# Optimization experiments

Measured on AMD Instinct MI355X. Metric: run time of the kernel, lower is better.

The kernel has to match this reference:

```python
import jax, jax.numpy as jnp
import numpy as np
import math

B, S, D = 2, 2048, 1024
H, KV, HD = 16, 4, 64
N_REP = H // KV
ROPE_THETA = 1.0e6


def _rope_tables(seq_len, head_dim, theta):
    inv_freq = 1.0 / (theta ** (np.arange(0, head_dim, 2, dtype=np.float32) / head_dim))
    t = np.arange(seq_len, dtype=np.float32)
    freqs = np.outer(t, inv_freq)                      # [S, HD/2]
    emb = np.concatenate([freqs, freqs], axis=-1)      # [S, HD]
    return jnp.asarray(np.cos(emb)), jnp.asarray(np.sin(emb))


def setup_inputs() -> dict:
    key = jax.random.key(0)
    ks = jax.random.split(key, 6)
    cos, sin = _rope_tables(S, HD, ROPE_THETA)
    scale = 0.02
    return {
        "x": jax.random.normal(ks[0], (B, S, D), dtype=jnp.float32),
        "cos": cos,
        "sin": sin,
        "Wq": jax.random.normal(ks[1], (D, H * HD), dtype=jnp.float32) * scale,
        "Wk": jax.random.normal(ks[2], (D, KV * HD), dtype=jnp.float32) * scale,
        "Wv": jax.random.normal(ks[3], (D, KV * HD), dtype=jnp.float32) * scale,
        "Wo": jax.random.normal(ks[4], (H * HD, D), dtype=jnp.float32) * scale,
    }


def _rotate_half(u):
    u1, u2 = u[..., : HD // 2], u[..., HD // 2 :]
    return jnp.concatenate([-u2, u1], axis=-1)


def reference(x, cos, sin, Wq, Wk, Wv, Wo):
    bsz, seq_len, _ = x.shape
    q = (x @ Wq).reshape(bsz, seq_len, H, HD)   # [B,S,H,HD]
    k = (x @ Wk).reshape(bsz, seq_len, KV, HD)  # [B,S,KV,HD]
    v = (x @ Wv).reshape(bsz, seq_len, KV, HD)

    # RoPE: cos/sin [S,HD] broadcast over batch and heads (unsqueeze_dim=1)
    c = cos[:seq_len][None, :, None, :]
    s = sin[:seq_len][None, :, None, :]
    q = q * c + _rotate_half(q) * s
    k = k * c + _rotate_half(k) * s

    # repeat_kv: expand KV heads groupwise to H heads
    k = jnp.repeat(k, N_REP, axis=2)  # [B,S,H,HD]
    v = jnp.repeat(v, N_REP, axis=2)

    q = q.transpose(0, 2, 1, 3)  # [B,H,S,HD]
    k = k.transpose(0, 2, 1, 3)
    v = v.transpose(0, 2, 1, 3)

    scores = jnp.einsum("bhqd,bhkd->bhqk", q, k) / math.sqrt(HD)
    causal = jnp.tril(jnp.ones((seq_len, seq_len), dtype=bool))
    scores = jnp.where(causal[None, None], scores, jnp.finfo(jnp.float32).min)
    probs = jax.nn.softmax(scores.astype(jnp.float32), axis=-1).astype(x.dtype)

    out = jnp.einsum("bhqk,bhkd->bhqd", probs, v)        # [B,H,S,HD]
    out = out.transpose(0, 2, 1, 3).reshape(bsz, seq_len, H * HD)
    return out @ Wo
```

## Files before the change

### kernel.cpp

```cpp
#include <hip/hip_runtime.h>

#define SS 2048
#define NH 16
#define NKV 4
#define HD 64

typedef __bf16 bf16;
typedef __bf16 bf16x4 __attribute__((ext_vector_type(4)));
typedef __bf16 bf16x8 __attribute__((ext_vector_type(8)));
typedef float f32x4 __attribute__((ext_vector_type(4)));

#define SM_SCALE 0.18033688011f

__device__ __forceinline__ void gl_lds16(const bf16* g, bf16* l) {
    __builtin_amdgcn_global_load_lds((const __attribute__((address_space(1))) void*)g,
                                     (__attribute__((address_space(3))) void*)l, 16, 0, 0);
}

__global__ __launch_bounds__(256) void prep_kernel(
    const float* __restrict__ x,
    const float* __restrict__ Wq, const float* __restrict__ Wk,
    const float* __restrict__ Wv, const float* __restrict__ Wo,
    bf16* __restrict__ wqkv_t, bf16* __restrict__ wo_t, bf16* __restrict__ xb)
{
    const int blk = blockIdx.x;
    const int tid = threadIdx.x;
    if (blk >= 640) {
        const size_t i0 = (size_t)(blk - 640) * 16384;
        #pragma unroll
        for (int i = 0; i < 16; ++i) {
            const size_t idx = i0 + i * 1024 + tid * 4;
            const float4 v = *(const float4*)&x[idx];
            bf16x4 o4;
            o4[0] = (bf16)v.x; o4[1] = (bf16)v.y; o4[2] = (bf16)v.z; o4[3] = (bf16)v.w;
            *(bf16x4*)&xb[idx] = o4;
        }
        return;
    }
    const float* W; bf16* Wt; int N, n0, k0;
    if (blk < 256)      { W = Wq; Wt = wqkv_t;                       N = 1024; n0 = (blk & 15) * 64;         k0 = (blk >> 4) * 64; }
    else if (blk < 320) { W = Wk; Wt = wqkv_t + (size_t)1024 * 1024; N = 256;  n0 = ((blk - 256) & 3) * 64;  k0 = ((blk - 256) >> 2) * 64; }
    else if (blk < 384) { W = Wv; Wt = wqkv_t + (size_t)1280 * 1024; N = 256;  n0 = ((blk - 320) & 3) * 64;  k0 = ((blk - 320) >> 2) * 64; }
    else                { W = Wo; Wt = wo_t;                         N = 1024; n0 = ((blk - 384) & 15) * 64; k0 = ((blk - 384) >> 4) * 64; }

    __shared__ float Ts[64][65];
    const int c = tid & 63, rr = tid >> 6;
    #pragma unroll
    for (int i = 0; i < 16; ++i) {
        const int kk = i * 4 + rr;
        Ts[kk][c] = W[(size_t)(k0 + kk) * N + n0 + c];
    }
    __syncthreads();
    #pragma unroll
    for (int i = 0; i < 16; ++i) {
        const int nn = i * 4 + rr;
        Wt[(size_t)(n0 + nn) * 1024 + k0 + c] = (bf16)Ts[c][nn];
    }
}

template<int EPI, int NBUF>
__global__ __launch_bounds__(256) void gemm_bt_kernel(
    const bf16* __restrict__ A, const bf16* __restrict__ Bt, float* __restrict__ C,
    const float* __restrict__ cosp, const float* __restrict__ sinp,
    bf16* __restrict__ qo, bf16* __restrict__ ko, bf16* __restrict__ vto,
    int N, int K, int CB)
{
    __shared__ bf16 As[NBUF][64 * 64];
    __shared__ bf16 Bs[NBUF][128 * 64];
    const int bid = blockIdx.x;
    const int j = bid >> 3;
    const int rb = (bid & 7) + 8 * (j / CB);
    const int cb = j % CB;
    const int m0 = rb * 64, n0 = cb * 128;
    const int tid = threadIdx.x;
    const int w = tid >> 6, lane = tid & 63, g = lane >> 4, li = lane & 15;
    const int wm = w >> 1, wn = w & 1;

    f32x4 acc[2][4];
    const f32x4 z = {0.f, 0.f, 0.f, 0.f};
    #pragma unroll
    for (int i = 0; i < 2; ++i)
        #pragma unroll
        for (int jj = 0; jj < 4; ++jj) acc[i][jj] = z;

    const int srow = tid >> 3;
    const int schunk = ((tid & 7) ^ (srow & 7)) * 8;
    const bf16* pA[2];
    const bf16* pB[4];
    #pragma unroll
    for (int s = 0; s < 2; ++s) pA[s] = A + (size_t)(m0 + s * 32 + srow) * K + schunk;
    #pragma unroll
    for (int s = 0; s < 4; ++s) pB[s] = Bt + (size_t)(n0 + s * 32 + srow) * K + schunk;
    const int lw = w * 512;

    const int NT = K >> 6;

    #pragma unroll
    for (int s = 0; s < 2; ++s) gl_lds16(pA[s], &As[0][s * 2048 + lw]);
    #pragma unroll
    for (int s = 0; s < 4; ++s) gl_lds16(pB[s], &Bs[0][s * 2048 + lw]);
    #pragma unroll
    for (int s = 0; s < 2; ++s) gl_lds16(pA[s] + 64, &As[1][s * 2048 + lw]);
    #pragma unroll
    for (int s = 0; s < 4; ++s) gl_lds16(pB[s] + 64, &Bs[1][s * 2048 + lw]);

    if (NBUF == 2) {
        for (int t = 0; t < NT; ++t) {
            const int cur = t & 1;
            if (t + 1 < NT) { asm volatile("s_waitcnt vmcnt(6)" ::: "memory"); }
            else            { asm volatile("s_waitcnt vmcnt(0)" ::: "memory"); }
            __builtin_amdgcn_s_barrier();
            #pragma unroll
            for (int tt = 0; tt < 2; ++tt) {
                const int phys = ((tt * 4 + g) ^ (li & 7)) * 8;
                bf16x8 af[2], bfr[4];
                #pragma unroll
                for (int mi = 0; mi < 2; ++mi) af[mi] = *(const bf16x8*)&As[cur][(wm * 32 + mi * 16 + li) * 64 + phys];
                #pragma unroll
                for (int ni = 0; ni < 4; ++ni) bfr[ni] = *(const bf16x8*)&Bs[cur][(wn * 64 + ni * 16 + li) * 64 + phys];
                __builtin_amdgcn_s_setprio(1);
                #pragma unroll
                for (int mi = 0; mi < 2; ++mi)
                    #pragma unroll
                    for (int ni = 0; ni < 4; ++ni)
                        acc[mi][ni] = __builtin_amdgcn_mfma_f32_16x16x32_bf16(af[mi], bfr[ni], acc[mi][ni], 0, 0, 0);
                __builtin_amdgcn_s_setprio(0);
            }
            __builtin_amdgcn_s_barrier();
            if (t + 2 < NT) {
                const int kk = (t + 2) << 6;
                #pragma unroll
                for (int s = 0; s < 2; ++s) gl_lds16(pA[s] + kk, &As[cur][s * 2048 + lw]);
                #pragma unroll
                for (int s = 0; s < 4; ++s) gl_lds16(pB[s] + kk, &Bs[cur][s * 2048 + lw]);
            }
        }
    } else {
        int cur = 0;
        for (int t = 0; t < NT; ++t) {
            if (t + 1 < NT) { asm volatile("s_waitcnt vmcnt(6)" ::: "memory"); }
            else            { asm volatile("s_waitcnt vmcnt(0)" ::: "memory"); }
            __builtin_amdgcn_s_barrier();
            if (t + 2 < NT) {
                const int kk = (t + 2) << 6;
                const int nb = (cur + 2 >= 3) ? cur - 1 : cur + 2;
                #pragma unroll
                for (int s = 0; s < 2; ++s) gl_lds16(pA[s] + kk, &As[nb][s * 2048 + lw]);
                #pragma unroll
                for (int s = 0; s < 4; ++s) gl_lds16(pB[s] + kk, &Bs[nb][s * 2048 + lw]);
            }
            #pragma unroll
            for (int tt = 0; tt < 2; ++tt) {
                const int phys = ((tt * 4 + g) ^ (li & 7)) * 8;
                bf16x8 af[2], bfr[4];
                #pragma unroll
                for (int mi = 0; mi < 2; ++mi) af[mi] = *(const bf16x8*)&As[cur][(wm * 32 + mi * 16 + li) * 64 + phys];
                #pragma unroll
                for (int ni = 0; ni < 4; ++ni) bfr[ni] = *(const bf16x8*)&Bs[cur][(wn * 64 + ni * 16 + li) * 64 + phys];
                __builtin_amdgcn_s_setprio(1);
                #pragma unroll
                for (int mi = 0; mi < 2; ++mi)
                    #pragma unroll
                    for (int ni = 0; ni < 4; ++ni)
                        acc[mi][ni] = __builtin_amdgcn_mfma_f32_16x16x32_bf16(af[mi], bfr[ni], acc[mi][ni], 0, 0, 0);
                __builtin_amdgcn_s_setprio(0);
            }
            cur = (cur + 1 == 3) ? 0 : cur + 1;
        }
    }

    const int row0 = m0 + wm * 32, col0 = n0 + wn * 64;
    if (EPI == 0) {
        #pragma unroll
        for (int mi = 0; mi < 2; ++mi)
            #pragma unroll
            for (int ni = 0; ni < 4; ++ni)
                #pragma unroll
                for (int r = 0; r < 4; ++r)
                    C[(size_t)(row0 + mi * 16 + g * 4 + r) * N + col0 + ni * 16 + li] = acc[mi][ni][r];
    } else {
        #pragma unroll
        for (int ni = 0; ni < 4; ++ni) {
            const int col = col0 + ni * 16 + li;
            const int d = col & 63;
            #pragma unroll
            for (int mi = 0; mi < 2; ++mi) {
                const int rowb = row0 + mi * 16 + g * 4;
                const int bb = rowb >> 11, s0 = rowb & 2047;
                if (col < 1280) {
                    #pragma unroll
                    for (int r = 0; r < 4; ++r) {
                        const int s = s0 + r;
                        float val = acc[mi][ni][r];
                        const float pairv = acc[mi][ni ^ 2][r];
                        const float rot = (d < 32) ? -pairv : pairv;
                        val = val * cosp[s * 64 + d] + rot * sinp[s * 64 + d];
                        if (col < 1024) {
                            const int hh = col >> 6;
                            qo[(((size_t)bb * NH + hh) * SS + s) * HD + d] = (bf16)(val * SM_SCALE);
                        } else {
                            const int kh = (col - 1024) >> 6;
                            ko[(((size_t)bb * NKV + kh) * SS + s) * HD + d] = (bf16)val;
                        }
                    }
                } else {
                    const int kh = (col - 1280) >> 6;
                    bf16x4 p4;
                    #pragma unroll
                    for (int r = 0; r < 4; ++r) p4[r] = (bf16)acc[mi][ni][r];
                    *(bf16x4*)&vto[(((size_t)bb * NKV + kh) * HD + d) * SS + s0] = p4;
                }
            }
        }
    }
}

__global__ __launch_bounds__(256) void flash_kernel(const bf16* __restrict__ q, const bf16* __restrict__ k,
                                                    const bf16* __restrict__ vt, bf16* __restrict__ o)
{
    __shared__ bf16 Ks[2][64 * 64];
    __shared__ bf16 Vt[2][64 * 64];
    __shared__ bf16 Ps[4][16 * 64];

    const int blk = blockIdx.x;
    const int qt = 31 - (blk >> 5);
    const int h = blk & 15;
    const int b = (blk >> 4) & 1;
    const int kvh = h >> 2;
    const int tid = threadIdx.x;
    const int w = tid >> 6, lane = tid & 63, g = lane >> 4, li = lane & 15;

    const bf16* qh = q + ((size_t)b * NH + h) * SS * HD;
    const bf16* kh = k + ((size_t)b * NKV + kvh) * SS * HD;
    const bf16* vh = vt + ((size_t)b * NKV + kvh) * (size_t)HD * SS;

    bf16x8 ones;
    #pragma unroll
    for (int jj = 0; jj < 8; ++jj) ones[jj] = (bf16)1.0f;
    const f32x4 z = {0.f, 0.f, 0.f, 0.f};

    const bf16* qrow = qh + (size_t)(qt * 64 + w * 16 + li) * HD;
    bf16x8 qf[2];
    qf[0] = *(const bf16x8*)(qrow + g * 8);
    qf[1] = *(const bf16x8*)(qrow + 32 + g * 8);

    const int srow = tid >> 3;
    const int schunk = ((tid & 7) ^ (srow & 7)) * 8;
    const int lw = w * 512;

    const int xm = (li & 7) << 1;

    f32x4 o_acc[4], l_acc;
    #pragma unroll
    for (int nt = 0; nt < 4; ++nt) o_acc[nt] = z;
    l_acc = z;

    #pragma unroll
    for (int s = 0; s < 2; ++s)
        gl_lds16(kh + (size_t)(s * 32 + srow) * HD + schunk, &Ks[0][s * 2048 + lw]);
    #pragma unroll
    for (int s = 0; s < 2; ++s)
        gl_lds16(vh + (size_t)(s * 32 + srow) * SS + schunk, &Vt[0][s * 2048 + lw]);
    if (qt >= 1) {
        #pragma unroll
        for (int s = 0; s < 2; ++s)
            gl_lds16(kh + (size_t)(64 + s * 32 + srow) * HD + schunk, &Ks[1][s * 2048 + lw]);
        #pragma unroll
        for (int s = 0; s < 2; ++s)
            gl_lds16(vh + (size_t)(s * 32 + srow) * SS + 64 + schunk, &Vt[1][s * 2048 + lw]);
    }

    for (int kt = 0; kt <= qt; ++kt) {
        const int cur = kt & 1;
        if (kt < qt) { asm volatile("s_waitcnt vmcnt(4)" ::: "memory"); }
        else         { asm volatile("s_waitcnt vmcnt(0)" ::: "memory"); }
        __builtin_amdgcn_s_barrier();

        f32x4 s_acc[4];
        #pragma unroll
        for (int nt = 0; nt < 4; ++nt) s_acc[nt] = z;
        __builtin_amdgcn_s_setprio(1);
        #pragma unroll
        for (int t = 0; t < 2; ++t)
            #pragma unroll
            for (int nt = 0; nt < 4; ++nt) {
                const bf16x8 kf = *(const bf16x8*)&Ks[cur][(nt * 16 + li) * 64 + (((t * 4 + g) ^ (li & 7)) * 8)];
                s_acc[nt] = __builtin_amdgcn_mfma_f32_16x16x32_bf16(kf, qf[t], s_acc[nt], 0, 0, 0);
            }
        __builtin_amdgcn_s_setprio(0);

        if (kt == qt) {
            const int qrow_in = w * 16 + li;
            #pragma unroll
            for (int nt = 0; nt < 4; ++nt) {
                bf16x4 p4;
                #pragma unroll
                for (int r = 0; r < 4; ++r) {
                    float sv = s_acc[nt][r];
                    if (nt * 16 + g * 4 + r > qrow_in) sv = -1e30f;
                    p4[r] = (bf16)exp2f(sv);
                }
                *(bf16x4*)&Ps[w][li * 64 + (((nt * 4 + g) ^ xm) * 4)] = p4;
            }
        } else {
            #pragma unroll
            for (int nt = 0; nt < 4; ++nt) {
                bf16x4 p4;
                #pragma unroll
                for (int r = 0; r < 4; ++r) p4[r] = (bf16)exp2f(s_acc[nt][r]);
                *(bf16x4*)&Ps[w][li * 64 + (((nt * 4 + g) ^ xm) * 4)] = p4;
            }
        }

        __builtin_amdgcn_s_setprio(1);
        #pragma unroll
        for (int t = 0; t < 2; ++t) {
            const bf16x8 pf = *(const bf16x8*)&Ps[w][li * 64 + (((t * 8 + g * 2) ^ xm) * 4)];
            l_acc = __builtin_amdgcn_mfma_f32_16x16x32_bf16(pf, ones, l_acc, 0, 0, 0);
            #pragma unroll
            for (int nt = 0; nt < 4; ++nt) {
                const bf16x8 vf = *(const bf16x8*)&Vt[cur][(nt * 16 + li) * 64 + (((t * 4 + g) ^ (li & 7)) * 8)];
                o_acc[nt] = __builtin_amdgcn_mfma_f32_16x16x32_bf16(pf, vf, o_acc[nt], 0, 0, 0);
            }
        }
        __builtin_amdgcn_s_setprio(0);

        __builtin_amdgcn_s_barrier();
        if (kt + 2 <= qt) {
            const size_t kq = (size_t)(kt + 2) * 64;
            #pragma unroll
            for (int s = 0; s < 2; ++s)
                gl_lds16(kh + (kq + s * 32 + srow) * HD + schunk, &Ks[cur][s * 2048 + lw]);
            #pragma unroll
            for (int s = 0; s < 2; ++s)
                gl_lds16(vh + (size_t)(s * 32 + srow) * SS + kq + schunk, &Vt[cur][s * 2048 + lw]);
        }
    }

    #pragma unroll
    for (int r = 0; r < 4; ++r) {
        const float inv = 1.f / l_acc[r];
        const int s = qt * 64 + w * 16 + g * 4 + r;
        bf16* orow = o + (((size_t)b * SS + s) * NH + h) * HD;
        #pragma unroll
        for (int nt = 0; nt < 4; ++nt) orow[nt * 16 + li] = (bf16)(o_acc[nt][r] * inv);
    }
}

extern "C" void kernel_launch(void* const* d_in, const int* in_sizes, int n_in,
                              void* d_out, int out_size, void* d_ws, size_t ws_size,
                              hipStream_t stream) {
    const float* x     = (const float*)d_in[0];
    const float* cos_t = (const float*)d_in[1];
    const float* sin_t = (const float*)d_in[2];
    const float* Wq    = (const float*)d_in[3];
    const float* Wk    = (const float*)d_in[4];
    const float* Wv    = (const float*)d_in[5];
    const float* Wo    = (const float*)d_in[6];
    float* out = (float*)d_out;

    char* wsb = (char*)d_ws;
    bf16* o_b    = (bf16*)(wsb);
    bf16* wqkv_t = (bf16*)(wsb + 8388608);
    bf16* wo_t   = (bf16*)(wsb + 11534336);
    bf16* q_b    = (bf16*)(wsb + 13631488);
    bf16* k_b    = (bf16*)(wsb + 22020096);
    bf16* vt_b   = (bf16*)(wsb + 24117248);
    bf16* x_b    = (bf16*)(wsb + 26214400);

    prep_kernel<<<896, 256, 0, stream>>>(x, Wq, Wk, Wv, Wo, wqkv_t, wo_t, x_b);

    gemm_bt_kernel<2, 2><<<768, 256, 0, stream>>>(x_b, wqkv_t, nullptr, cos_t, sin_t,
                                                  q_b, k_b, vt_b, 1536, 1024, 12);
    flash_kernel<<<1024, 256, 0, stream>>>(q_b, k_b, vt_b, o_b);
    gemm_bt_kernel<0, 3><<<512, 256, 0, stream>>>(o_b, wo_t, out, nullptr, nullptr,
                                                  nullptr, nullptr, nullptr, 1024, 1024, 8);
}
```

Baseline: 158.6 us.

## Split long causal query tiles across two KV halves with partial-sum reduce

The upper half of query tiles (qt 16..31) is split into two work units that each process half of the KV range and write unnormalized partial outputs and row sums to a workspace. A new reduce kernel combines the two halves and normalizes. A lookup table orders the units longest-first, so the critical path of the flash kernel is shorter and load balance across CUs improves. In exchange there is an extra kernel launch and extra fp32 partial traffic. The partials are combined without a running max, which relies on the kernel's existing no-max softmax scheme.

```diff
diff --git a/kernel.cpp b/kernel.cpp
--- a/kernel.cpp
+++ b/kernel.cpp
@@ -16,6 +16,11 @@
     __builtin_amdgcn_global_load_lds((const __attribute__((address_space(1))) void*)g,
                                      (__attribute__((address_space(3))) void*)l, 16, 0, 0);
 }
+
+__device__ const unsigned char unit_tab[48] = {
+    124, 125, 120, 62, 121, 116, 117, 112, 58, 113, 108, 109, 104, 54, 105, 100,
+    101, 96, 50, 97, 92, 93, 88, 46, 89, 84, 85, 80, 42, 81, 76, 77,
+    72, 38, 73, 68, 69, 64, 34, 65, 30, 26, 22, 18, 14, 10, 6, 2};
 
 __global__ __launch_bounds__(256) void prep_kernel(
     const float* __restrict__ x,
@@ -216,16 +221,22 @@
 }
 
 __global__ __launch_bounds__(256) void flash_kernel(const bf16* __restrict__ q, const bf16* __restrict__ k,
-                                                    const bf16* __restrict__ vt, bf16* __restrict__ o)
+                                                    const bf16* __restrict__ vt, bf16* __restrict__ o,
+                                                    float* __restrict__ part)
 {
     __shared__ bf16 Ks[2][64 * 64];
     __shared__ bf16 Vt[2][64 * 64];
     __shared__ bf16 Ps[4][16 * 64];
 
     const int blk = blockIdx.x;
-    const int qt = 31 - (blk >> 5);
-    const int h = blk & 15;
-    const int b = (blk >> 4) & 1;
+    const int u = blk >> 5, bh = blk & 31;
+    const int e = unit_tab[u];
+    const int qt = e >> 2, mode = e & 3;
+    const int khalf = (qt + 2) >> 1;
+    const int k0 = (mode == 1) ? khalf : 0;
+    const int k1 = (mode == 0) ? khalf : qt + 1;
+    const int h = bh & 15;
+    const int b = bh >> 4;
     const int kvh = h >> 2;
     const int tid = threadIdx.x;
     const int w = tid >> 6, lane = tid & 63, g = lane >> 4, li = lane & 15;
@@ -255,25 +266,26 @@
     for (int nt = 0; nt < 4; ++nt) o_acc[nt] = z;
     l_acc = z;
 
+    const int kb0 = k0 * 64;
     #pragma unroll
     for (int s = 0; s < 2; ++s)
-        gl_lds16(kh + (size_t)(s * 32 + srow) * HD + schunk, &Ks[0][s * 2048 + lw]);
+        gl_lds16(kh + (size_t)(kb0 + s * 32 + srow) * HD + schunk, &Ks[0][s * 2048 + lw]);
     #pragma unroll
     for (int s = 0; s < 2; ++s)
-        gl_lds16(vh + (size_t)(s * 32 + srow) * SS + schunk, &Vt[0][s * 2048 + lw]);
-    if (qt >= 1) {
+        gl_lds16(vh + (size_t)(s * 32 + srow) * SS + kb0 + schunk, &Vt[0][s * 2048 + lw]);
+    if (k0 + 1 < k1) {
         #pragma unroll
         for (int s = 0; s < 2; ++s)
-            gl_lds16(kh + (size_t)(64 + s * 32 + srow) * HD + schunk, &Ks[1][s * 2048 + lw]);
+            gl_lds16(kh + (size_t)(kb0 + 64 + s * 32 + srow) * HD + schunk, &Ks[1][s * 2048 + lw]);
         #pragma unroll
         for (int s = 0; s < 2; ++s)
-            gl_lds16(vh + (size_t)(s * 32 + srow) * SS + 64 + schunk, &Vt[1][s * 2048 + lw]);
-    }
-
-    for (int kt = 0; kt <= qt; ++kt) {
-        const int cur = kt & 1;
-        if (kt < qt) { asm volatile("s_waitcnt vmcnt(4)" ::: "memory"); }
-        else         { asm volatile("s_waitcnt vmcnt(0)" ::: "memory"); }
+            gl_lds16(vh + (size_t)(s * 32 + srow) * SS + kb0 + 64 + schunk, &Vt[1][s * 2048 + lw]);
+    }
+
+    for (int kt = k0; kt < k1; ++kt) {
+        const int cur = (kt - k0) & 1;
+        if (kt + 1 < k1) { asm volatile("s_waitcnt vmcnt(4)" ::: "memory"); }
+        else             { asm volatile("s_waitcnt vmcnt(0)" ::: "memory"); }
         __builtin_amdgcn_s_barrier();
 
         f32x4 s_acc[4];
@@ -326,7 +338,7 @@
         __builtin_amdgcn_s_setprio(0);
 
         __builtin_amdgcn_s_barrier();
-        if (kt + 2 <= qt) {
+        if (kt + 2 < k1) {
             const size_t kq = (size_t)(kt + 2) * 64;
             #pragma unroll
             for (int s = 0; s < 2; ++s)
@@ -337,14 +349,63 @@
         }
     }
 
-    #pragma unroll
-    for (int r = 0; r < 4; ++r) {
-        const float inv = 1.f / l_acc[r];
-        const int s = qt * 64 + w * 16 + g * 4 + r;
-        bf16* orow = o + (((size_t)b * SS + s) * NH + h) * HD;
-        #pragma unroll
-        for (int nt = 0; nt < 4; ++nt) orow[nt * 16 + li] = (bf16)(o_acc[nt][r] * inv);
-    }
+    if (mode == 2) {
+        #pragma unroll
+        for (int r = 0; r < 4; ++r) {
+            const float inv = 1.f / l_acc[r];
+            const int s = qt * 64 + w * 16 + g * 4 + r;
+            bf16* orow = o + (((size_t)b * SS + s) * NH + h) * HD;
+            #pragma unroll
+            for (int nt = 0; nt < 4; ++nt) orow[nt * 16 + li] = (bf16)(o_acc[nt][r] * inv);
+        }
+    } else {
+        float* PO = part + (size_t)((bh * 16 + (qt - 16)) * 2 + mode) * 4160;
+        float* PL = PO + 4096;
+        #pragma unroll
+        for (int r = 0; r < 4; ++r) {
+            const int row = w * 16 + g * 4 + r;
+            #pragma unroll
+            for (int nt = 0; nt < 4; ++nt) PO[row * 64 + nt * 16 + li] = o_acc[nt][r];
+            if (li == 0) PL[row] = l_acc[r];
+        }
+    }
+}
+
+__global__ __launch_bounds__(256) void reduce_kernel(const float* __restrict__ part,
+                                                     bf16* __restrict__ o)
+{
+    const int rb = blockIdx.x;
+    const int bh = rb >> 4, sq = rb & 15;
+    const int qt = 16 + sq;
+    const int b = bh >> 4, h = bh & 15;
+    const int tid = threadIdx.x;
+    const int row = tid >> 2, c0 = (tid & 3) << 4;
+    const float* P0 = part + (size_t)((bh * 16 + sq) * 2) * 4160;
+    const float* P1 = P0 + 4160;
+    const float inv = 1.f / (P0[4096 + row] + P1[4096 + row]);
+    const int s = qt * 64 + row;
+    bf16* orow = o + (((size_t)b * SS + s) * NH + h) * HD + c0;
+    const float4* a = (const float4*)&P0[row * 64 + c0];
+    const float4* c = (const float4*)&P1[row * 64 + c0];
+    bf16x8 v0, v1;
+    #pragma unroll
+    for (int i = 0; i < 2; ++i) {
+        const float4 s0 = a[i], s1 = c[i];
+        v0[i * 4 + 0] = (bf16)((s0.x + s1.x) * inv);
+        v0[i * 4 + 1] = (bf16)((s0.y + s1.y) * inv);
+        v0[i * 4 + 2] = (bf16)((s0.z + s1.z) * inv);
+        v0[i * 4 + 3] = (bf16)((s0.w + s1.w) * inv);
+    }
+    #pragma unroll
+    for (int i = 0; i < 2; ++i) {
+        const float4 s0 = a[2 + i], s1 = c[2 + i];
+        v1[i * 4 + 0] = (bf16)((s0.x + s1.x) * inv);
+        v1[i * 4 + 1] = (bf16)((s0.y + s1.y) * inv);
+        v1[i * 4 + 2] = (bf16)((s0.z + s1.z) * inv);
+        v1[i * 4 + 3] = (bf16)((s0.w + s1.w) * inv);
+    }
+    *(bf16x8*)orow = v0;
+    *(bf16x8*)(orow + 8) = v1;
 }
 
 extern "C" void kernel_launch(void* const* d_in, const int* in_sizes, int n_in,
@@ -367,12 +428,14 @@
     bf16* k_b    = (bf16*)(wsb + 22020096);
     bf16* vt_b   = (bf16*)(wsb + 24117248);
     bf16* x_b    = (bf16*)(wsb + 26214400);
+    float* part  = (float*)(wsb + 34603008);
 
     prep_kernel<<<896, 256, 0, stream>>>(x, Wq, Wk, Wv, Wo, wqkv_t, wo_t, x_b);
 
     gemm_bt_kernel<2, 2><<<768, 256, 0, stream>>>(x_b, wqkv_t, nullptr, cos_t, sin_t,
                                                   q_b, k_b, vt_b, 1536, 1024, 12);
-    flash_kernel<<<1024, 256, 0, stream>>>(q_b, k_b, vt_b, o_b);
+    flash_kernel<<<1536, 256, 0, stream>>>(q_b, k_b, vt_b, o_b, part);
+    reduce_kernel<<<512, 256, 0, stream>>>(part, o_b);
     gemm_bt_kernel<0, 3><<<512, 256, 0, stream>>>(o_b, wo_t, out, nullptr, nullptr,
                                                   nullptr, nullptr, nullptr, 1024, 1024, 8);
 }
```

New measurement: 161.9 us. 2.0% more time.
